# Kernel optimization log

Measured on AMD Instinct MI355X. Metric: run time of the kernel, lower is better.

Reference implementation:

```python
import jax, jax.numpy as jnp
import numpy as np

N, E, L, D_IN = 20000, 320000, 3, 128
K, H = 8, 64
NEG_SLOPE = 0.01


def setup_inputs() -> dict:
    key = jax.random.key(0)
    k1, k2, k3, k4, k5, k6 = jax.random.split(key, 6)
    return {
        "node_feat": jax.random.normal(k1, (N, D_IN), jnp.float32),
        "edge_feat": jax.random.normal(k2, (E, L, D_IN), jnp.float32),
        "W_enc": jax.random.normal(k3, (D_IN, K * H), jnp.float32) * (1.0 / np.sqrt(D_IN)),
        "attn_l": jax.random.normal(k4, (1, K, H), jnp.float32) * 0.1,
        "W_r": jax.random.normal(k5, (K, D_IN), jnp.float32) * (1.0 / np.sqrt(D_IN)),
        "dst": jax.random.randint(k6, (E,), 0, N, jnp.int32),
    }


def reference(node_feat, edge_feat, W_enc, attn_l, W_r, dst):
    n = node_feat.shape[0]
    e_cnt = edge_feat.shape[0]
    # metapath instance encoder ('linear'): mean over metapath length, then project
    ft = jnp.mean(edge_feat, axis=1) @ W_enc            # (E, K*H)
    ft = ft.reshape(e_cnt, K, H)                        # (E, K, H)
    # per-edge / per-dst attention logits
    el = jnp.sum(ft * attn_l, axis=-1)                  # (E, K)
    er = node_feat @ W_r.T                              # (N, K)
    e = jax.nn.leaky_relu(el + er[dst], negative_slope=NEG_SLOPE)  # (E, K)
    # edge_softmax: segmented (per destination node) stable softmax
    seg_max = jax.ops.segment_max(e, dst, num_segments=n)
    seg_max = jnp.where(jnp.isfinite(seg_max), seg_max, 0.0)
    ex = jnp.exp(e - seg_max[dst])                      # (E, K)
    seg_sum = jax.ops.segment_sum(ex, dst, num_segments=n)
    a = ex / seg_sum[dst]                               # (E, K)  (attn_drop=0 in eval)
    # weighted scatter-sum of edge features into destination nodes
    out = jax.ops.segment_sum(ft * a[..., None], dst, num_segments=n)  # (N, K, H)
    return out
```

## Files before the change

kernel.cpp:

```cpp
#include <hip/hip_runtime.h>
#include <math.h>

#define NN   20000
#define EE   320000
#define DIN  128
#define KK   8
#define HH   64
#define NEG  0.01f

typedef __attribute__((ext_vector_type(8))) short short8;
typedef __attribute__((ext_vector_type(4))) float f32x4;

__device__ __forceinline__ unsigned short f2bf(float f) {
  unsigned u = __float_as_uint(f);
  u += 0x7FFF + ((u >> 16) & 1);
  return (unsigned short)(u >> 16);
}
__device__ __forceinline__ float bf2f_lo(unsigned u) {
  return __uint_as_float(u << 16);
}
__device__ __forceinline__ float bf2f_hi(unsigned u) {
  return __uint_as_float(u & 0xFFFF0000u);
}

__device__ __forceinline__ float wave_sum(float v) {
#pragma unroll
  for (int m = 1; m < 64; m <<= 1) v += __shfl_xor(v, m, 64);
  return v;
}

__global__ __launch_bounds__(256) void k_vt(const float* __restrict__ W_enc,
                                            const float* __restrict__ attn_l,
                                            unsigned short* __restrict__ Vt) {
  int gid = blockIdx.x * 256 + threadIdx.x;
  if (gid >= 16 * 128) return;
  int n = gid >> 7, d = gid & 127;
  float acc = 0.f;
  if (n < 8) {
#pragma unroll 8
    for (int h = 0; h < HH; ++h)
      acc += W_enc[(size_t)d * 512 + n * 64 + h] * attn_l[n * 64 + h];
  }
  Vt[gid] = f2bf(acc);
}

__global__ __launch_bounds__(256) void k_wt(const float* __restrict__ W_enc,
                                            unsigned short* __restrict__ Wt) {
  int gid = blockIdx.x * 256 + threadIdx.x;
  int row = gid >> 7, d = gid & 127;
  Wt[gid] = f2bf(W_enc[(size_t)d * 512 + row]);
}

__global__ __launch_bounds__(256) void k_er(const float* __restrict__ node_feat,
                                            const float* __restrict__ W_r,
                                            float* __restrict__ er) {
  __shared__ __align__(16) float4 wr4[KK * 32];
  int tid = threadIdx.x;
  if (tid < 256) wr4[tid] = ((const float4*)W_r)[tid];
  __syncthreads();
  int gid = blockIdx.x * 256 + tid;
  int n = gid >> 3, k = gid & 7;
  if (n < NN) {
    const float4* nf4 = (const float4*)node_feat + (size_t)n * 32;
    float acc = 0.f;
#pragma unroll
    for (int i = 0; i < 32; ++i) {
      float4 a = nf4[i], b = wr4[k * 32 + i];
      acc += a.x * b.x + a.y * b.y + a.z * b.z + a.w * b.w;
    }
    er[gid] = acc;
  }
}

__global__ __launch_bounds__(256) void k_mean(const float* __restrict__ ef,
                                              unsigned short* __restrict__ x) {
  size_t gid = (size_t)blockIdx.x * 256 + threadIdx.x;
  size_t e = gid >> 4;
  int s = gid & 15;
  const float4* p = (const float4*)(ef + e * 384) + s * 2;
  float4 a0 = p[0],  a1 = p[1];
  float4 b0 = p[32], b1 = p[33];
  float4 c0 = p[64], c1 = p[65];
  const float i3 = 1.f / 3.f;
  float m0 = (a0.x + b0.x + c0.x) * i3, m1 = (a0.y + b0.y + c0.y) * i3;
  float m2 = (a0.z + b0.z + c0.z) * i3, m3 = (a0.w + b0.w + c0.w) * i3;
  float m4 = (a1.x + b1.x + c1.x) * i3, m5 = (a1.y + b1.y + c1.y) * i3;
  float m6 = (a1.z + b1.z + c1.z) * i3, m7 = (a1.w + b1.w + c1.w) * i3;
  uint4 o;
  o.x = (unsigned)f2bf(m0) | ((unsigned)f2bf(m1) << 16);
  o.y = (unsigned)f2bf(m2) | ((unsigned)f2bf(m3) << 16);
  o.z = (unsigned)f2bf(m4) | ((unsigned)f2bf(m5) << 16);
  o.w = (unsigned)f2bf(m6) | ((unsigned)f2bf(m7) << 16);
  ((uint4*)x)[gid] = o;
}

__global__ __launch_bounds__(256) void k_logit(const unsigned short* __restrict__ x,
                                               const unsigned short* __restrict__ Vt,
                                               const float* __restrict__ er,
                                               const int* __restrict__ dst,
                                               float* __restrict__ e_log,
                                               int* __restrict__ counts) {
  int lane = threadIdx.x & 63;
  int gw = (blockIdx.x * 256 + (int)threadIdx.x) >> 6;
  int e0 = gw * 16;
  int m = lane & 15, quad = lane >> 4;
  const short8* xr = (const short8*)(x + (size_t)(e0 + m) * 128);
  const short8* vr = (const short8*)(Vt + (size_t)m * 128);
  f32x4 acc = {0.f, 0.f, 0.f, 0.f};
#pragma unroll
  for (int kt = 0; kt < 4; ++kt) {
    short8 a = xr[kt * 4 + quad];
    short8 b = vr[kt * 4 + quad];
    acc = __builtin_amdgcn_mfma_f32_16x16x32_bf16(a, b, acc, 0, 0, 0);
  }
  if (m < 8) {
#pragma unroll
    for (int r = 0; r < 4; ++r) {
      int e = e0 + quad * 4 + r;
      int dv = dst[e];
      float z = acc[r] + er[dv * 8 + m];
      z = z > 0.f ? z : NEG * z;
      e_log[(size_t)e * 8 + m] = z;
      if (m == 0) atomicAdd(&counts[dv], 1);
    }
  }
}

__device__ __forceinline__ int block_excl_scan256(int v, int tid) {
  __shared__ int wtot[4];
  int lane = tid & 63, wid = tid >> 6;
  int incl = v;
#pragma unroll
  for (int off = 1; off < 64; off <<= 1) {
    int t = __shfl_up(incl, off, 64);
    if (lane >= off) incl += t;
  }
  if (lane == 63) wtot[wid] = incl;
  __syncthreads();
  if (tid == 0) {
    int s = 0;
#pragma unroll
    for (int i = 0; i < 4; ++i) { int t = wtot[i]; wtot[i] = s; s += t; }
  }
  __syncthreads();
  return wtot[wid] + incl - v;
}

__global__ __launch_bounds__(256) void k_scan1(const int* __restrict__ counts,
                                               int* __restrict__ lexcl,
                                               int* __restrict__ btot) {
  int b = blockIdx.x, tid = threadIdx.x;
  int i = b * 256 + tid;
  int v = (i < NN) ? counts[i] : 0;
  int ex = block_excl_scan256(v, tid);
  lexcl[i] = ex;
  if (tid == 255) btot[b] = ex + v;
}

__global__ __launch_bounds__(256) void k_scan2(int* __restrict__ btot,
                                               int* __restrict__ bbase,
                                               int* __restrict__ offs) {
  int tid = threadIdx.x;
  int v = (tid < 80) ? btot[tid] : 0;
  int ex = block_excl_scan256(v, tid);
  if (tid < 80) bbase[tid] = ex;
  if (tid == 0) offs[NN] = EE;
}

__global__ __launch_bounds__(256) void k_scan3(const int* __restrict__ lexcl,
                                               const int* __restrict__ bbase,
                                               int* __restrict__ offs,
                                               int* __restrict__ cursor) {
  int b = blockIdx.x, tid = threadIdx.x;
  int i = b * 256 + tid;
  if (i < NN) {
    int o = lexcl[i] + bbase[b];
    offs[i] = o;
    cursor[i] = o;
  }
}

__global__ __launch_bounds__(256) void k_fill(const int* __restrict__ dst,
                                              int* __restrict__ cursor,
                                              int* __restrict__ elist) {
  int e = blockIdx.x * 256 + threadIdx.x;
  if (e < EE) {
    int p = atomicAdd(&cursor[dst[e]], 1);
    elist[p] = e;
  }
}

__global__ __launch_bounds__(256) void k_agg(const int* __restrict__ offs,
                                             const int* __restrict__ elist,
                                             const float* __restrict__ e_log,
                                             const unsigned short* __restrict__ x,
                                             unsigned short* __restrict__ y) {
  __shared__ float maxs[8], invs[8];
  __shared__ float red[4][8];
  __shared__ __align__(16) float xs[32 * 128];
  __shared__ __align__(16) float wbuf[32 * 8];
  int n = blockIdx.x;
  int tid = threadIdx.x, lane = tid & 63, wid = tid >> 6;
  int start = offs[n], end = offs[n + 1];

  float m[8];
#pragma unroll
  for (int k = 0; k < 8; ++k) m[k] = -3.4e38f;
  for (int i = start + tid; i < end; i += 256) {
    size_t e = (size_t)elist[i];
    float4 a = ((const float4*)e_log)[e * 2 + 0];
    float4 b = ((const float4*)e_log)[e * 2 + 1];
    m[0] = fmaxf(m[0], a.x); m[1] = fmaxf(m[1], a.y);
    m[2] = fmaxf(m[2], a.z); m[3] = fmaxf(m[3], a.w);
    m[4] = fmaxf(m[4], b.x); m[5] = fmaxf(m[5], b.y);
    m[6] = fmaxf(m[6], b.z); m[7] = fmaxf(m[7], b.w);
  }
#pragma unroll
  for (int k = 0; k < 8; ++k) {
#pragma unroll
    for (int mm = 1; mm < 64; mm <<= 1) m[k] = fmaxf(m[k], __shfl_xor(m[k], mm, 64));
  }
  if (lane == 0) {
#pragma unroll
    for (int k = 0; k < 8; ++k) red[wid][k] = m[k];
  }
  __syncthreads();
  if (tid < 8)
    maxs[tid] = fmaxf(fmaxf(red[0][tid], red[1][tid]), fmaxf(red[2][tid], red[3][tid]));
  __syncthreads();
  float mk[8];
#pragma unroll
  for (int k = 0; k < 8; ++k) mk[k] = maxs[k];

  float s[8];
#pragma unroll
  for (int k = 0; k < 8; ++k) s[k] = 0.f;
  for (int i = start + tid; i < end; i += 256) {
    size_t e = (size_t)elist[i];
    float4 a = ((const float4*)e_log)[e * 2 + 0];
    float4 b = ((const float4*)e_log)[e * 2 + 1];
    s[0] += __expf(a.x - mk[0]); s[1] += __expf(a.y - mk[1]);
    s[2] += __expf(a.z - mk[2]); s[3] += __expf(a.w - mk[3]);
    s[4] += __expf(b.x - mk[4]); s[5] += __expf(b.y - mk[5]);
    s[6] += __expf(b.z - mk[6]); s[7] += __expf(b.w - mk[7]);
  }
#pragma unroll
  for (int k = 0; k < 8; ++k) s[k] = wave_sum(s[k]);
  if (lane == 0) {
#pragma unroll
    for (int k = 0; k < 8; ++k) red[wid][k] = s[k];
  }
  __syncthreads();
  if (tid < 8) {
    float tot = red[0][tid] + red[1][tid] + red[2][tid] + red[3][tid];
    invs[tid] = tot > 0.f ? 1.f / tot : 0.f;
  }
  __syncthreads();

  float acc0 = 0.f, acc1 = 0.f, acc2 = 0.f, acc3 = 0.f;
  int d = tid & 127, kg = tid >> 7;
  for (int base = start; base < end; base += 32) {
    int nb = min(32, end - base);
    for (int j = tid; j < nb * 16; j += 256) {
      size_t e = (size_t)elist[base + (j >> 4)];
      uint4 t = ((const uint4*)x)[e * 16 + (j & 15)];
      float4 lo = make_float4(bf2f_lo(t.x), bf2f_hi(t.x), bf2f_lo(t.y), bf2f_hi(t.y));
      float4 hi = make_float4(bf2f_lo(t.z), bf2f_hi(t.z), bf2f_lo(t.w), bf2f_hi(t.w));
      ((float4*)xs)[(j >> 4) * 32 + (j & 15) * 2 + 0] = lo;
      ((float4*)xs)[(j >> 4) * 32 + (j & 15) * 2 + 1] = hi;
    }
    if (tid < nb * 8) {
      size_t e = (size_t)elist[base + (tid >> 3)];
      int k = tid & 7;
      wbuf[tid] = __expf(e_log[e * 8 + k] - maxs[k]) * invs[k];
    }
    __syncthreads();
    for (int j = 0; j < nb; ++j) {
      float xv = xs[j * 128 + d];
      float4 wv = *(const float4*)&wbuf[j * 8 + kg * 4];
      acc0 += wv.x * xv; acc1 += wv.y * xv; acc2 += wv.z * xv; acc3 += wv.w * xv;
    }
    __syncthreads();
  }
  size_t yb = ((size_t)n * 8 + kg * 4) * 128 + d;
  y[yb + 0 * 128] = f2bf(acc0);
  y[yb + 1 * 128] = f2bf(acc1);
  y[yb + 2 * 128] = f2bf(acc2);
  y[yb + 3 * 128] = f2bf(acc3);
}

__global__ __launch_bounds__(256) void k_out(const unsigned short* __restrict__ y,
                                             const unsigned short* __restrict__ Wt,
                                             float* __restrict__ out) {
  int kh = blockIdx.y;
  int n0 = blockIdx.x * 16;
  int wv = threadIdx.x >> 6;
  int lane = threadIdx.x & 63;
  int m = lane & 15, quad = lane >> 4;
  int h0 = wv * 16;
  const short8* ar = (const short8*)(y + ((size_t)(n0 + m) * 8 + kh) * 128);
  const short8* br = (const short8*)(Wt + (size_t)(kh * 64 + h0 + m) * 128);
  f32x4 acc = {0.f, 0.f, 0.f, 0.f};
#pragma unroll
  for (int kt = 0; kt < 4; ++kt) {
    short8 a = ar[kt * 4 + quad];
    short8 b = br[kt * 4 + quad];
    acc = __builtin_amdgcn_mfma_f32_16x16x32_bf16(a, b, acc, 0, 0, 0);
  }
#pragma unroll
  for (int r = 0; r < 4; ++r)
    out[(size_t)(n0 + quad * 4 + r) * 512 + kh * 64 + h0 + m] = acc[r];
}

extern "C" void kernel_launch(void* const* d_in, const int* in_sizes, int n_in,
                              void* d_out, int out_size, void* d_ws, size_t ws_size,
                              hipStream_t stream) {
  const float* node_feat = (const float*)d_in[0];
  const float* edge_feat = (const float*)d_in[1];
  const float* W_enc     = (const float*)d_in[2];
  const float* attn_l    = (const float*)d_in[3];
  const float* W_r       = (const float*)d_in[4];
  const int*   dst       = (const int*)d_in[5];
  float* out = (float*)d_out;

  char* ws = (char*)d_ws;
  size_t off = 0;
  auto carve = [&](size_t bytes) {
    void* p = ws + off;
    off = (off + bytes + 255) & ~(size_t)255;
    return p;
  };
  unsigned short* x   = (unsigned short*)carve((size_t)EE * DIN * 2);
  unsigned short* y   = (unsigned short*)carve((size_t)NN * KK * DIN * 2);
  unsigned short* Vt  = (unsigned short*)carve(16 * 128 * 2);
  unsigned short* Wt  = (unsigned short*)carve((size_t)KK * HH * DIN * 2);
  float* er    = (float*)carve((size_t)NN * KK * 4);
  float* e_log = (float*)carve((size_t)EE * KK * 4);
  int* counts  = (int*)carve((size_t)20480 * 4);
  int* lexcl   = (int*)carve((size_t)20480 * 4);
  int* btot    = (int*)carve(80 * 4);
  int* bbase   = (int*)carve(80 * 4);
  int* offs    = (int*)carve((size_t)(NN + 1) * 4);
  int* cursor  = (int*)carve((size_t)NN * 4);
  int* elist   = (int*)carve((size_t)EE * 4);
  (void)ws_size; (void)in_sizes; (void)n_in; (void)out_size;

  hipMemsetAsync(counts, 0, (size_t)NN * 4, stream);

  k_vt  <<<8, 256, 0, stream>>>(W_enc, attn_l, Vt);
  k_wt  <<<256, 256, 0, stream>>>(W_enc, Wt);
  k_er  <<<(NN * KK) / 256, 256, 0, stream>>>(node_feat, W_r, er);
  k_mean<<<(EE * 16) / 256, 256, 0, stream>>>(edge_feat, x);
  k_logit<<<EE / 64, 256, 0, stream>>>(x, Vt, er, dst, e_log, counts);
  k_scan1<<<80, 256, 0, stream>>>(counts, lexcl, btot);
  k_scan2<<<1, 256, 0, stream>>>(btot, bbase, offs);
  k_scan3<<<80, 256, 0, stream>>>(lexcl, bbase, offs, cursor);
  k_fill<<<EE / 256, 256, 0, stream>>>(dst, cursor, elist);
  k_agg <<<NN, 256, 0, stream>>>(offs, elist, e_log, x, y);
  k_out <<<dim3(NN / 16, KK), 256, 0, stream>>>(y, Wt, out);
}
```

Baseline: 872.7 us.

## Fuse precompute kernels, fuse mean with logit MFMA, cache softmax weights in LDS

Merges the three small precompute kernels (Vt, Wt, er) into one launch and fuses the edge-feature mean with the logit MFMA, so the bf16 x tile is consumed from shared memory and not re-read from global. In the aggregation kernel, nodes with at most 128 in-edges load their edge ids and logits into shared memory once and compute max, exp, sum and normalise there. This replaces three passes of gathered global reads, and nodes above the cap keep the old path. The costs are a larger shared-memory footprint per block in k_agg, which can lower occupancy, and only one of four waves doing MFMA work in k_mlog.

```diff
diff --git a/kernel.cpp b/kernel.cpp
--- a/kernel.cpp
+++ b/kernel.cpp
@@ -7,6 +7,7 @@
 #define KK   8
 #define HH   64
 #define NEG  0.01f
+#define CAP  128
 
 typedef __attribute__((ext_vector_type(8))) short short8;
 typedef __attribute__((ext_vector_type(4))) float f32x4;
@@ -29,52 +30,57 @@
   return v;
 }
 
-__global__ __launch_bounds__(256) void k_vt(const float* __restrict__ W_enc,
-                                            const float* __restrict__ attn_l,
-                                            unsigned short* __restrict__ Vt) {
-  int gid = blockIdx.x * 256 + threadIdx.x;
-  if (gid >= 16 * 128) return;
-  int n = gid >> 7, d = gid & 127;
-  float acc = 0.f;
-  if (n < 8) {
+__global__ __launch_bounds__(256) void k_pre(const float* __restrict__ W_enc,
+                                             const float* __restrict__ attn_l,
+                                             const float* __restrict__ node_feat,
+                                             const float* __restrict__ W_r,
+                                             unsigned short* __restrict__ Wt,
+                                             unsigned short* __restrict__ Vt,
+                                             float* __restrict__ er) {
+  __shared__ __align__(16) float4 wr4[KK * 32];
+  int b = blockIdx.x, tid = threadIdx.x;
+  if (b < 256) {
+    int gid = b * 256 + tid;
+    int row = gid >> 7, d = gid & 127;
+    Wt[gid] = f2bf(W_enc[(size_t)d * 512 + row]);
+  } else if (b < 264) {
+    int gid = (b - 256) * 256 + tid;
+    int n = gid >> 7, d = gid & 127;
+    float acc = 0.f;
+    if (n < 8) {
 #pragma unroll 8
-    for (int h = 0; h < HH; ++h)
-      acc += W_enc[(size_t)d * 512 + n * 64 + h] * attn_l[n * 64 + h];
-  }
-  Vt[gid] = f2bf(acc);
-}
-
-__global__ __launch_bounds__(256) void k_wt(const float* __restrict__ W_enc,
-                                            unsigned short* __restrict__ Wt) {
-  int gid = blockIdx.x * 256 + threadIdx.x;
-  int row = gid >> 7, d = gid & 127;
-  Wt[gid] = f2bf(W_enc[(size_t)d * 512 + row]);
-}
-
-__global__ __launch_bounds__(256) void k_er(const float* __restrict__ node_feat,
-                                            const float* __restrict__ W_r,
-                                            float* __restrict__ er) {
-  __shared__ __align__(16) float4 wr4[KK * 32];
+      for (int h = 0; h < HH; ++h)
+        acc += W_enc[(size_t)d * 512 + n * 64 + h] * attn_l[n * 64 + h];
+    }
+    Vt[gid] = f2bf(acc);
+  } else {
+    wr4[tid] = ((const float4*)W_r)[tid];
+    __syncthreads();
+    int gid = (b - 264) * 256 + tid;
+    int n = gid >> 3, k = gid & 7;
+    if (n < NN) {
+      const float4* nf4 = (const float4*)node_feat + (size_t)n * 32;
+      float acc = 0.f;
+#pragma unroll
+      for (int i = 0; i < 32; ++i) {
+        float4 a = nf4[i], bb = wr4[k * 32 + i];
+        acc += a.x * bb.x + a.y * bb.y + a.z * bb.z + a.w * bb.w;
+      }
+      er[gid] = acc;
+    }
+  }
+}
+
+__global__ __launch_bounds__(256) void k_mlog(const float* __restrict__ ef,
+                                              const unsigned short* __restrict__ Vt,
+                                              const float* __restrict__ er,
+                                              const int* __restrict__ dst,
+                                              unsigned short* __restrict__ x,
+                                              float* __restrict__ e_log,
+                                              int* __restrict__ counts) {
+  __shared__ __align__(16) uint4 xl4[16 * 17];
   int tid = threadIdx.x;
-  if (tid < 256) wr4[tid] = ((const float4*)W_r)[tid];
-  __syncthreads();
-  int gid = blockIdx.x * 256 + tid;
-  int n = gid >> 3, k = gid & 7;
-  if (n < NN) {
-    const float4* nf4 = (const float4*)node_feat + (size_t)n * 32;
-    float acc = 0.f;
-#pragma unroll
-    for (int i = 0; i < 32; ++i) {
-      float4 a = nf4[i], b = wr4[k * 32 + i];
-      acc += a.x * b.x + a.y * b.y + a.z * b.z + a.w * b.w;
-    }
-    er[gid] = acc;
-  }
-}
-
-__global__ __launch_bounds__(256) void k_mean(const float* __restrict__ ef,
-                                              unsigned short* __restrict__ x) {
-  size_t gid = (size_t)blockIdx.x * 256 + threadIdx.x;
+  size_t gid = (size_t)blockIdx.x * 256 + tid;
   size_t e = gid >> 4;
   int s = gid & 15;
   const float4* p = (const float4*)(ef + e * 384) + s * 2;
@@ -92,36 +98,32 @@
   o.z = (unsigned)f2bf(m4) | ((unsigned)f2bf(m5) << 16);
   o.w = (unsigned)f2bf(m6) | ((unsigned)f2bf(m7) << 16);
   ((uint4*)x)[gid] = o;
-}
-
-__global__ __launch_bounds__(256) void k_logit(const unsigned short* __restrict__ x,
-                                               const unsigned short* __restrict__ Vt,
-                                               const float* __restrict__ er,
-                                               const int* __restrict__ dst,
-                                               float* __restrict__ e_log,
-                                               int* __restrict__ counts) {
-  int lane = threadIdx.x & 63;
-  int gw = (blockIdx.x * 256 + (int)threadIdx.x) >> 6;
-  int e0 = gw * 16;
-  int m = lane & 15, quad = lane >> 4;
-  const short8* xr = (const short8*)(x + (size_t)(e0 + m) * 128);
-  const short8* vr = (const short8*)(Vt + (size_t)m * 128);
-  f32x4 acc = {0.f, 0.f, 0.f, 0.f};
-#pragma unroll
-  for (int kt = 0; kt < 4; ++kt) {
-    short8 a = xr[kt * 4 + quad];
-    short8 b = vr[kt * 4 + quad];
-    acc = __builtin_amdgcn_mfma_f32_16x16x32_bf16(a, b, acc, 0, 0, 0);
-  }
-  if (m < 8) {
-#pragma unroll
-    for (int r = 0; r < 4; ++r) {
-      int e = e0 + quad * 4 + r;
-      int dv = dst[e];
-      float z = acc[r] + er[dv * 8 + m];
-      z = z > 0.f ? z : NEG * z;
-      e_log[(size_t)e * 8 + m] = z;
-      if (m == 0) atomicAdd(&counts[dv], 1);
+  xl4[(tid >> 4) * 17 + (tid & 15)] = o;
+  __syncthreads();
+
+  if (tid < 64) {
+    int lane = tid;
+    int m = lane & 15, quad = lane >> 4;
+    size_t e0 = (size_t)blockIdx.x * 16;
+    const short8* xr = (const short8*)((const unsigned short*)xl4 + m * 136);
+    const short8* vr = (const short8*)(Vt + (size_t)m * 128);
+    f32x4 acc = {0.f, 0.f, 0.f, 0.f};
+#pragma unroll
+    for (int kt = 0; kt < 4; ++kt) {
+      short8 a = xr[kt * 4 + quad];
+      short8 bfr = vr[kt * 4 + quad];
+      acc = __builtin_amdgcn_mfma_f32_16x16x32_bf16(a, bfr, acc, 0, 0, 0);
+    }
+    if (m < 8) {
+#pragma unroll
+      for (int r = 0; r < 4; ++r) {
+        size_t ee = e0 + quad * 4 + r;
+        int dv = dst[ee];
+        float z = acc[r] + er[(size_t)dv * 8 + m];
+        z = z > 0.f ? z : NEG * z;
+        e_log[ee * 8 + m] = z;
+        if (m == 0) atomicAdd(&counts[dv], 1);
+      }
     }
   }
 }
@@ -195,93 +197,155 @@
                                              const float* __restrict__ e_log,
                                              const unsigned short* __restrict__ x,
                                              unsigned short* __restrict__ y) {
+  __shared__ float red[4][8];
   __shared__ float maxs[8], invs[8];
-  __shared__ float red[4][8];
+  __shared__ int eids[CAP];
+  __shared__ __align__(16) float w[CAP * 8];
   __shared__ __align__(16) float xs[32 * 128];
-  __shared__ __align__(16) float wbuf[32 * 8];
   int n = blockIdx.x;
   int tid = threadIdx.x, lane = tid & 63, wid = tid >> 6;
   int start = offs[n], end = offs[n + 1];
-
-  float m[8];
-#pragma unroll
-  for (int k = 0; k < 8; ++k) m[k] = -3.4e38f;
-  for (int i = start + tid; i < end; i += 256) {
-    size_t e = (size_t)elist[i];
-    float4 a = ((const float4*)e_log)[e * 2 + 0];
-    float4 b = ((const float4*)e_log)[e * 2 + 1];
-    m[0] = fmaxf(m[0], a.x); m[1] = fmaxf(m[1], a.y);
-    m[2] = fmaxf(m[2], a.z); m[3] = fmaxf(m[3], a.w);
-    m[4] = fmaxf(m[4], b.x); m[5] = fmaxf(m[5], b.y);
-    m[6] = fmaxf(m[6], b.z); m[7] = fmaxf(m[7], b.w);
-  }
-#pragma unroll
-  for (int k = 0; k < 8; ++k) {
-#pragma unroll
-    for (int mm = 1; mm < 64; mm <<= 1) m[k] = fmaxf(m[k], __shfl_xor(m[k], mm, 64));
-  }
-  if (lane == 0) {
-#pragma unroll
-    for (int k = 0; k < 8; ++k) red[wid][k] = m[k];
-  }
-  __syncthreads();
-  if (tid < 8)
-    maxs[tid] = fmaxf(fmaxf(red[0][tid], red[1][tid]), fmaxf(red[2][tid], red[3][tid]));
-  __syncthreads();
-  float mk[8];
-#pragma unroll
-  for (int k = 0; k < 8; ++k) mk[k] = maxs[k];
-
-  float s[8];
-#pragma unroll
-  for (int k = 0; k < 8; ++k) s[k] = 0.f;
-  for (int i = start + tid; i < end; i += 256) {
-    size_t e = (size_t)elist[i];
-    float4 a = ((const float4*)e_log)[e * 2 + 0];
-    float4 b = ((const float4*)e_log)[e * 2 + 1];
-    s[0] += __expf(a.x - mk[0]); s[1] += __expf(a.y - mk[1]);
-    s[2] += __expf(a.z - mk[2]); s[3] += __expf(a.w - mk[3]);
-    s[4] += __expf(b.x - mk[4]); s[5] += __expf(b.y - mk[5]);
-    s[6] += __expf(b.z - mk[6]); s[7] += __expf(b.w - mk[7]);
-  }
-#pragma unroll
-  for (int k = 0; k < 8; ++k) s[k] = wave_sum(s[k]);
-  if (lane == 0) {
-#pragma unroll
-    for (int k = 0; k < 8; ++k) red[wid][k] = s[k];
-  }
-  __syncthreads();
-  if (tid < 8) {
-    float tot = red[0][tid] + red[1][tid] + red[2][tid] + red[3][tid];
-    invs[tid] = tot > 0.f ? 1.f / tot : 0.f;
-  }
-  __syncthreads();
-
+  int cnt = end - start;
+  int d = tid & 127, kg = tid >> 7;
   float acc0 = 0.f, acc1 = 0.f, acc2 = 0.f, acc3 = 0.f;
-  int d = tid & 127, kg = tid >> 7;
-  for (int base = start; base < end; base += 32) {
-    int nb = min(32, end - base);
-    for (int j = tid; j < nb * 16; j += 256) {
-      size_t e = (size_t)elist[base + (j >> 4)];
-      uint4 t = ((const uint4*)x)[e * 16 + (j & 15)];
-      float4 lo = make_float4(bf2f_lo(t.x), bf2f_hi(t.x), bf2f_lo(t.y), bf2f_hi(t.y));
-      float4 hi = make_float4(bf2f_lo(t.z), bf2f_hi(t.z), bf2f_lo(t.w), bf2f_hi(t.w));
-      ((float4*)xs)[(j >> 4) * 32 + (j & 15) * 2 + 0] = lo;
-      ((float4*)xs)[(j >> 4) * 32 + (j & 15) * 2 + 1] = hi;
-    }
-    if (tid < nb * 8) {
-      size_t e = (size_t)elist[base + (tid >> 3)];
-      int k = tid & 7;
-      wbuf[tid] = __expf(e_log[e * 8 + k] - maxs[k]) * invs[k];
-    }
-    __syncthreads();
-    for (int j = 0; j < nb; ++j) {
-      float xv = xs[j * 128 + d];
-      float4 wv = *(const float4*)&wbuf[j * 8 + kg * 4];
-      acc0 += wv.x * xv; acc1 += wv.y * xv; acc2 += wv.z * xv; acc3 += wv.w * xv;
-    }
-    __syncthreads();
-  }
+
+  if (cnt <= CAP) {
+    for (int i = tid; i < cnt; i += 256) eids[i] = elist[start + i];
+    __syncthreads();
+    for (int j = tid; j < cnt * 2; j += 256)
+      ((float4*)w)[j] = ((const float4*)e_log)[(size_t)eids[j >> 1] * 2 + (j & 1)];
+    __syncthreads();
+
+    int k = tid & 7, ib = tid >> 3;
+    float mm = -3.4e38f;
+    for (int i = ib; i < cnt; i += 32) mm = fmaxf(mm, w[i * 8 + k]);
+    mm = fmaxf(mm, __shfl_xor(mm, 8, 64));
+    mm = fmaxf(mm, __shfl_xor(mm, 16, 64));
+    mm = fmaxf(mm, __shfl_xor(mm, 32, 64));
+    if ((lane >> 3) == 0) red[wid][lane] = mm;
+    __syncthreads();
+    if (tid < 8)
+      maxs[tid] = fmaxf(fmaxf(red[0][tid], red[1][tid]), fmaxf(red[2][tid], red[3][tid]));
+    __syncthreads();
+
+    float mk = maxs[k];
+    float ss = 0.f;
+    for (int i = ib; i < cnt; i += 32) {
+      float v = __expf(w[i * 8 + k] - mk);
+      w[i * 8 + k] = v;
+      ss += v;
+    }
+    ss += __shfl_xor(ss, 8, 64);
+    ss += __shfl_xor(ss, 16, 64);
+    ss += __shfl_xor(ss, 32, 64);
+    if ((lane >> 3) == 0) red[wid][lane] = ss;
+    __syncthreads();
+    if (tid < 8) {
+      float tot = red[0][tid] + red[1][tid] + red[2][tid] + red[3][tid];
+      invs[tid] = tot > 0.f ? 1.f / tot : 0.f;
+    }
+    __syncthreads();
+    float iv = invs[k];
+    for (int i = ib; i < cnt; i += 32) w[i * 8 + k] *= iv;
+    __syncthreads();
+
+    for (int base = 0; base < cnt; base += 32) {
+      int nb = min(32, cnt - base);
+      for (int j = tid; j < nb * 16; j += 256) {
+        size_t e = (size_t)eids[base + (j >> 4)];
+        uint4 t = ((const uint4*)x)[e * 16 + (j & 15)];
+        float4 lo = make_float4(bf2f_lo(t.x), bf2f_hi(t.x), bf2f_lo(t.y), bf2f_hi(t.y));
+        float4 hi = make_float4(bf2f_lo(t.z), bf2f_hi(t.z), bf2f_lo(t.w), bf2f_hi(t.w));
+        ((float4*)xs)[(j >> 4) * 32 + (j & 15) * 2 + 0] = lo;
+        ((float4*)xs)[(j >> 4) * 32 + (j & 15) * 2 + 1] = hi;
+      }
+      __syncthreads();
+      for (int j = 0; j < nb; ++j) {
+        float xv = xs[j * 128 + d];
+        const float* wp = &w[(base + j) * 8 + kg * 4];
+        acc0 += wp[0] * xv; acc1 += wp[1] * xv; acc2 += wp[2] * xv; acc3 += wp[3] * xv;
+      }
+      __syncthreads();
+    }
+  } else {
+    float m8[8];
+#pragma unroll
+    for (int k = 0; k < 8; ++k) m8[k] = -3.4e38f;
+    for (int i = start + tid; i < end; i += 256) {
+      size_t e = (size_t)elist[i];
+      float4 a = ((const float4*)e_log)[e * 2 + 0];
+      float4 b = ((const float4*)e_log)[e * 2 + 1];
+      m8[0] = fmaxf(m8[0], a.x); m8[1] = fmaxf(m8[1], a.y);
+      m8[2] = fmaxf(m8[2], a.z); m8[3] = fmaxf(m8[3], a.w);
+      m8[4] = fmaxf(m8[4], b.x); m8[5] = fmaxf(m8[5], b.y);
+      m8[6] = fmaxf(m8[6], b.z); m8[7] = fmaxf(m8[7], b.w);
+    }
+#pragma unroll
+    for (int k = 0; k < 8; ++k) {
+#pragma unroll
+      for (int mm2 = 1; mm2 < 64; mm2 <<= 1)
+        m8[k] = fmaxf(m8[k], __shfl_xor(m8[k], mm2, 64));
+    }
+    if (lane == 0) {
+#pragma unroll
+      for (int k = 0; k < 8; ++k) red[wid][k] = m8[k];
+    }
+    __syncthreads();
+    if (tid < 8)
+      maxs[tid] = fmaxf(fmaxf(red[0][tid], red[1][tid]), fmaxf(red[2][tid], red[3][tid]));
+    __syncthreads();
+    float mk8[8];
+#pragma unroll
+    for (int k = 0; k < 8; ++k) mk8[k] = maxs[k];
+    float s8[8];
+#pragma unroll
+    for (int k = 0; k < 8; ++k) s8[k] = 0.f;
+    for (int i = start + tid; i < end; i += 256) {
+      size_t e = (size_t)elist[i];
+      float4 a = ((const float4*)e_log)[e * 2 + 0];
+      float4 b = ((const float4*)e_log)[e * 2 + 1];
+      s8[0] += __expf(a.x - mk8[0]); s8[1] += __expf(a.y - mk8[1]);
+      s8[2] += __expf(a.z - mk8[2]); s8[3] += __expf(a.w - mk8[3]);
+      s8[4] += __expf(b.x - mk8[4]); s8[5] += __expf(b.y - mk8[5]);
+      s8[6] += __expf(b.z - mk8[6]); s8[7] += __expf(b.w - mk8[7]);
+    }
+#pragma unroll
+    for (int k = 0; k < 8; ++k) s8[k] = wave_sum(s8[k]);
+    if (lane == 0) {
+#pragma unroll
+      for (int k = 0; k < 8; ++k) red[wid][k] = s8[k];
+    }
+    __syncthreads();
+    if (tid < 8) {
+      float tot = red[0][tid] + red[1][tid] + red[2][tid] + red[3][tid];
+      invs[tid] = tot > 0.f ? 1.f / tot : 0.f;
+    }
+    __syncthreads();
+    for (int base = start; base < end; base += 32) {
+      int nb = min(32, end - base);
+      for (int j = tid; j < nb * 16; j += 256) {
+        size_t e = (size_t)elist[base + (j >> 4)];
+        uint4 t = ((const uint4*)x)[e * 16 + (j & 15)];
+        float4 lo = make_float4(bf2f_lo(t.x), bf2f_hi(t.x), bf2f_lo(t.y), bf2f_hi(t.y));
+        float4 hi = make_float4(bf2f_lo(t.z), bf2f_hi(t.z), bf2f_lo(t.w), bf2f_hi(t.w));
+        ((float4*)xs)[(j >> 4) * 32 + (j & 15) * 2 + 0] = lo;
+        ((float4*)xs)[(j >> 4) * 32 + (j & 15) * 2 + 1] = hi;
+      }
+      if (tid < nb * 8) {
+        size_t e = (size_t)elist[base + (tid >> 3)];
+        int kk = tid & 7;
+        w[tid] = __expf(e_log[e * 8 + kk] - maxs[kk]) * invs[kk];
+      }
+      __syncthreads();
+      for (int j = 0; j < nb; ++j) {
+        float xv = xs[j * 128 + d];
+        float4 wv = *(const float4*)&w[j * 8 + kg * 4];
+        acc0 += wv.x * xv; acc1 += wv.y * xv; acc2 += wv.z * xv; acc3 += wv.w * xv;
+      }
+      __syncthreads();
+    }
+  }
+
   size_t yb = ((size_t)n * 8 + kg * 4) * 128 + d;
   y[yb + 0 * 128] = f2bf(acc0);
   y[yb + 1 * 128] = f2bf(acc1);
@@ -347,11 +411,9 @@
 
   hipMemsetAsync(counts, 0, (size_t)NN * 4, stream);
 
-  k_vt  <<<8, 256, 0, stream>>>(W_enc, attn_l, Vt);
-  k_wt  <<<256, 256, 0, stream>>>(W_enc, Wt);
-  k_er  <<<(NN * KK) / 256, 256, 0, stream>>>(node_feat, W_r, er);
-  k_mean<<<(EE * 16) / 256, 256, 0, stream>>>(edge_feat, x);
-  k_logit<<<EE / 64, 256, 0, stream>>>(x, Vt, er, dst, e_log, counts);
+  k_pre <<<264 + (NN * KK) / 256, 256, 0, stream>>>(W_enc, attn_l, node_feat, W_r,
+                                                    Wt, Vt, er);
+  k_mlog<<<(EE * 16) / 256, 256, 0, stream>>>(edge_feat, Vt, er, dst, x, e_log, counts);
   k_scan1<<<80, 256, 0, stream>>>(counts, lexcl, btot);
   k_scan2<<<1, 256, 0, stream>>>(btot, bbase, offs);
   k_scan3<<<80, 256, 0, stream>>>(lexcl, bbase, offs, cursor);
```

Measured after the change: 786.7 us. -9.9%, faster.
